# Kernel tuning notes

Hardware: AMD Instinct MI355X
Metric: run time of the kernel (lower is better)

The kernel has to match this reference:

```python
import jax, jax.numpy as jnp
from jax import lax
import numpy as np

B, C, O, NF, H, W = 4, 64, 64, 64, 128, 128
DK = 3
K = DK * DK
PAD = DK // 2


def setup_inputs() -> dict:
    key = jax.random.key(0)
    k0, k1, k2, k3 = jax.random.split(key, 4)
    inputs = jax.random.normal(k0, (B, C, H, W), jnp.float32)
    feat = jax.random.normal(k1, (B, NF, H, W), jnp.float32)
    # small offset-conv weights keep learned offsets in a realistic sub-pixel range
    om_w = jax.random.normal(k2, (C * 3 * K, NF, 3, 3), jnp.float32) * 0.02
    om_b = jnp.zeros((C * 3 * K,), jnp.float32)
    dc_w = jax.random.normal(k3, (O, C, DK, DK), jnp.float32) * (1.0 / np.sqrt(C * K))
    dc_b = jnp.zeros((O,), jnp.float32)
    return dict(inputs=inputs, feat=feat, om_w=om_w, om_b=om_b, dc_w=dc_w, dc_b=dc_b)


def _gather(img, y, x):
    # img: [B,C,H,W]; y,x: int32 [B,C,K,H,W]; zero outside bounds
    valid = (y >= 0) & (y < H) & (x >= 0) & (x < W)
    yc = jnp.clip(y, 0, H - 1)
    xc = jnp.clip(x, 0, W - 1)
    idx = (yc * W + xc).reshape(B, C, K, H * W)
    flat = img.reshape(B, C, 1, H * W)
    v = jnp.take_along_axis(flat, idx, axis=3).reshape(B, C, K, H, W)
    return jnp.where(valid, v, 0.0)


def _forward(inputs, feat, om_w, om_b, dc_w, dc_b):
    # offset/mask conv: nf -> in_nc*3*K, 3x3, pad 1
    off_msk = lax.conv_general_dilated(
        feat, om_w, (1, 1), ((1, 1), (1, 1)),
        dimension_numbers=('NCHW', 'OIHW', 'NCHW')) + om_b[None, :, None, None]
    # offsets interleaved (y,x) per kernel tap per deformable group (= channel)
    off = off_msk[:, :C * 2 * K].reshape(B, C, K, 2, H, W)
    msk = jax.nn.sigmoid(off_msk[:, C * 2 * K:]).reshape(B, C, K, H, W)

    ky = (jnp.arange(K) // DK - PAD).astype(jnp.float32)  # [K]
    kx = (jnp.arange(K) % DK - PAD).astype(jnp.float32)
    hg = jnp.arange(H, dtype=jnp.float32)
    wg = jnp.arange(W, dtype=jnp.float32)
    py = hg[None, None, None, :, None] + ky[None, None, :, None, None] + off[:, :, :, 0]  # [B,C,K,H,W]
    px = wg[None, None, None, None, :] + kx[None, None, :, None, None] + off[:, :, :, 1]

    y0f = jnp.floor(py); x0f = jnp.floor(px)
    wy = py - y0f; wx = px - x0f
    y0 = y0f.astype(jnp.int32); x0 = x0f.astype(jnp.int32)
    y1 = y0 + 1; x1 = x0 + 1

    v00 = _gather(inputs, y0, x0)
    v01 = _gather(inputs, y0, x1)
    v10 = _gather(inputs, y1, x0)
    v11 = _gather(inputs, y1, x1)
    sampled = ((1 - wy) * (1 - wx) * v00 + (1 - wy) * wx * v01
               + wy * (1 - wx) * v10 + wy * wx * v11) * msk  # [B,C,K,H,W]

    out = jnp.einsum('bckhw,ock->bohw', sampled, dc_w.reshape(O, C, K))
    out = out + dc_b[None, :, None, None]
    return jax.nn.relu(out)


def reference(inputs, feat, om_w, om_b, dc_w, dc_b):
    return _forward(inputs, feat, om_w, om_b, dc_w, dc_b)
```

## Files before the change

kernel.cpp:

```cpp
#include <hip/hip_runtime.h>
#include <hip/hip_bf16.h>

typedef __bf16 bf16;
typedef __bf16 bf16x8 __attribute__((ext_vector_type(8)));
typedef __bf16 bf16x4 __attribute__((ext_vector_type(4)));
typedef float f32x4 __attribute__((ext_vector_type(4)));
typedef float f32x2 __attribute__((ext_vector_type(2)));
typedef float f32x2u __attribute__((ext_vector_type(2))) __attribute__((aligned(4)));
typedef int  i32x4 __attribute__((ext_vector_type(4)));

#define MFMA16(a, b, c) __builtin_amdgcn_mfma_f32_16x16x32_bf16((a), (b), (c), 0, 0, 0)

static constexpr size_t FEATS_OFF = 0;
static constexpr size_t OMW3_OFF  = 8388608;
static constexpr size_t DCW_OFF   = OMW3_OFF + 1990656;
static constexpr size_t SC_OFF    = DCW_OFF + 73728;
static constexpr size_t PAD_OFF   = SC_OFF + 9216;


__global__ void prep_featS(const float* __restrict__ feat, bf16* __restrict__ featS) {
    const int hh = blockIdx.x, b = blockIdx.y;
    __shared__ float t[64][129];
    for (int i = threadIdx.x; i < 64 * 32; i += 256) {
        int cf = i >> 5, q = i & 31;
        const float* src = feat + ((size_t)(b * 64 + cf) * 128 + hh) * 128 + q * 4;
        t[cf][q * 4 + 0] = src[0];
        t[cf][q * 4 + 1] = src[1];
        t[cf][q * 4 + 2] = src[2];
        t[cf][q * 4 + 3] = src[3];
    }
    __syncthreads();
    for (int i = threadIdx.x; i < 1024; i += 256) {
        int px = i >> 3, cfb = i & 7;
        int sb = cfb ^ (px & 7);
        bf16x8 v;
#pragma unroll
        for (int e = 0; e < 8; ++e) v[e] = (bf16)t[cfb * 8 + e][px];
        *(bf16x8*)(featS + ((size_t)((b * 128 + hh) * 128 + px) << 6) + sb * 8) = v;
    }
}

__global__ void prep_weights(const float* __restrict__ om_w, const float* __restrict__ om_b,
                             const float* __restrict__ dc_w,
                             bf16* __restrict__ omw3, bf16* __restrict__ dcw2p,
                             float* __restrict__ scf) {
    int i = blockIdx.x * 256 + threadIdx.x;
    if (i < 995328) {
        int e = i & 511, lane = e >> 3, j = e & 7;
        int q = i >> 9;
        int t = q % 3, q2 = q / 3, kk = q2 % 18, ct = q2 / 18;
        int ck = ct * 16 + (lane & 15);
        int kcol = kk * 32 + (lane >> 4) * 8 + j;
        int tap = kcol >> 6, cf = kcol & 63;
        int ch = (t < 2) ? (ck * 2 + t) : (1152 + ck);
        omw3[i] = (bf16)om_w[ch * 576 + cf * 9 + tap];
    }
    if (i < 36864) {
        int j = i & 7, lane = (i >> 3) & 63, ot = (i >> 9) & 3, win = i >> 11;
        int o = ot * 16 + (lane & 15);
        int ck = win * 32 + (lane >> 4) * 8 + j;
        dcw2p[i] = (bf16)dc_w[o * 576 + ck];
    }
    if (i < 576) {
        int ck = i;
        int c = ck / 9, kd = ck - 9 * c, kq = kd / 3, kx = kd - 3 * kq;
        int pr = ck >> 1, lo = ck & 1;
        scf[pr * 8 + 0 + lo] = om_b[ck * 2]     + (float)(kq + 2);
        scf[pr * 8 + 2 + lo] = om_b[ck * 2 + 1] + (float)(kx + 2);
        scf[pr * 8 + 4 + lo] = om_b[1152 + ck];
        scf[pr * 8 + 6 + lo] = __uint_as_float((unsigned)(c * 17956));
    }
}

__global__ void prep_pad(const float* __restrict__ inputs, float* __restrict__ pad) {
    int yy = blockIdx.x, bc = blockIdx.y, xx = threadIdx.x;
    if (xx >= 134) return;
    float v = 0.f;
    if (yy >= 3 && yy <= 130 && xx >= 3 && xx <= 130)
        v = inputs[(size_t)bc * 16384 + (yy - 3) * 128 + (xx - 3)];
    pad[((size_t)bc * 134 + yy) * 134 + xx] = v;
}


__global__ void __launch_bounds__(256, 3)
deform_fused(const float* __restrict__ pad,
             const bf16* __restrict__ featS,
             const bf16* __restrict__ omw3,
             const bf16* __restrict__ dcw2p,
             const f32x4* __restrict__ sconst,
             const float* __restrict__ dcb,
             float* __restrict__ out)
{
    const int bid = blockIdx.x;
    const int P0 = (bid & 1) << 6;
    const int h = (bid >> 1) & 127;
    const int b = bid >> 8;
    const int tid = threadIdx.x;
    const int lane = tid & 63;
    const int wid_s = __builtin_amdgcn_readfirstlane(tid >> 6);
    const int l15 = lane & 15, g = lane >> 4;

    __shared__ __align__(16) unsigned char smem[41728];
    char* featB = (char*)smem;
    char* bufA  = (char*)smem + 25344;
    char* bufB  = (char*)smem + 33536;

    for (int i = tid; i < 6336; i += 256) ((unsigned*)featB)[i] = 0u;
    __syncthreads();
    {
        const int s0 = (P0 == 0) ? 0 : 63;
        const int q0 = (P0 == 0) ? 1 : 0;
        for (int i = tid; i < 1560; i += 256) {
            int ky = i / 520, rem = i - ky * 520, row = rem >> 3, c = rem & 7;
            int hh = h - 1 + ky;
            if ((unsigned)hh < 128u) {
                const char* src = (const char*)featS
                    + (((size_t)(b * 128 + hh) * 128 + s0 + row) << 7) + c * 16;
                *(i32x4*)(featB + ((ky * 66 + q0 + row) << 7) + c * 16) = *(const i32x4*)src;
            }
        }
    }
    __syncthreads();

    int fb9[9];
#pragma unroll
    for (int tap = 0; tap < 9; ++tap) {
        const int kyp = tap / 3, kxp = tap - 3 * kyp;
        const int q = l15 + kxp;
        fb9[tap] = (kyp * 66 + q) * 128 + ((g ^ ((q + 7) & 7)) << 4);
    }

    f32x4 acc2[4];
#pragma unroll
    for (int u = 0; u < 4; ++u) acc2[u] = (f32x4){0.f, 0.f, 0.f, 0.f};

    const bf16* omw3_l = omw3 + lane * 8;
    const bf16* dcw_l  = dcw2p + lane * 8;
    const float* padb0 = pad + (size_t)b * 64 * 17956;
    const f32x2 hb2 = {(float)h, (float)h};
    const f32x2 fx2 = {(float)(P0 + l15), (float)(P0 + l15)};
    const int g4 = g * 4;
    const int rswz = (g ^ (l15 & 7)) << 4;
    const int wswz = ((wid_s * 4 + g) ^ ((l15 & 7) << 1)) << 3;

#pragma unroll 1
    for (int blk = 0; blk < 9; ++blk) {
        char* bcur  = (blk & 1) ? bufB : bufA;
        char* bprev = (blk & 1) ? bufA : bufB;

        if (blk > 0) {
            bf16x8 aK0 = *(const bf16x8*)(dcw_l + (((blk - 1) * 8 + wid_s) << 9));
            bf16x8 aK1 = *(const bf16x8*)(dcw_l + (((blk - 1) * 8 + 4 + wid_s) << 9));
            __builtin_amdgcn_s_setprio(1);
#pragma unroll
            for (int u = 0; u < 4; ++u) {
                const int rb = (u * 16 + l15) * 128 + rswz;
                bf16x8 b0 = *(const bf16x8*)(bprev + rb);
                bf16x8 b1 = *(const bf16x8*)(bprev + (rb ^ 64));
                acc2[u] = MFMA16(aK0, b0, acc2[u]);
                acc2[u] = MFMA16(aK1, b1, acc2[u]);
            }
            __builtin_amdgcn_s_setprio(0);
        }

        f32x4 acc1[3][4];
#pragma unroll
        for (int t = 0; t < 3; ++t)
#pragma unroll
            for (int nf = 0; nf < 4; ++nf) acc1[t][nf] = (f32x4){0.f, 0.f, 0.f, 0.f};

        const int abase = (blk * 4 + wid_s) * 27648;
#pragma unroll
        for (int kk = 0; kk < 18; ++kk) {
            bf16x8 a0 = *(const bf16x8*)(omw3_l + abase + ((kk * 3 + 0) << 9));
            bf16x8 a1 = *(const bf16x8*)(omw3_l + abase + ((kk * 3 + 1) << 9));
            bf16x8 a2 = *(const bf16x8*)(omw3_l + abase + ((kk * 3 + 2) << 9));
            const int base = fb9[kk >> 1] ^ ((kk & 1) << 6);
            bf16x8 bfr[4];
#pragma unroll
            for (int nf = 0; nf < 4; ++nf)
                bfr[nf] = *(const bf16x8*)(featB + base + nf * 2048);
            __builtin_amdgcn_s_setprio(1);
#pragma unroll
            for (int nf = 0; nf < 4; ++nf) {
                acc1[0][nf] = MFMA16(a0, bfr[nf], acc1[0][nf]);
                acc1[1][nf] = MFMA16(a1, bfr[nf], acc1[1][nf]);
                acc1[2][nf] = MFMA16(a2, bfr[nf], acc1[2][nf]);
            }
            __builtin_amdgcn_s_setprio(0);
        }

        const f32x4* scB = sconst + (blk * 64 + wid_s * 16);
        f32x4 e0A = scB[g4 + 0], e1A = scB[g4 + 1];
        f32x4 e0B = scB[g4 + 2], e1B = scB[g4 + 3];
        f32x2 yb[2], xb[2], mb[2];
        unsigned co[2][2];
        yb[0] = f32x2{e0A.x, e0A.y} + hb2;
        xb[0] = f32x2{e0A.z, e0A.w} + fx2;
        mb[0] = f32x2{e1A.x, e1A.y};
        co[0][0] = __float_as_uint(e1A.z); co[0][1] = __float_as_uint(e1A.w);
        yb[1] = f32x2{e0B.x, e0B.y} + hb2;
        xb[1] = f32x2{e0B.z, e0B.w} + fx2;
        mb[1] = f32x2{e1B.x, e1B.y};
        co[1][0] = __float_as_uint(e1B.z); co[1][1] = __float_as_uint(e1B.w);

#pragma unroll
        for (int nf = 0; nf < 4; ++nf) {
            float s[4];
#pragma unroll
            for (int pi = 0; pi < 2; ++pi) {
                f32x2 py = f32x2{acc1[0][nf][2 * pi], acc1[0][nf][2 * pi + 1]} + yb[pi];
                f32x2 px = f32x2{acc1[1][nf][2 * pi], acc1[1][nf][2 * pi + 1]} + xb[pi];
                f32x2 lg = f32x2{acc1[2][nf][2 * pi], acc1[2][nf][2 * pi + 1]} + mb[pi];
#pragma unroll
                for (int e = 0; e < 2; ++e) {
                    float pyc = __builtin_amdgcn_fmed3f(py[e], 0.5f, 132.5f);
                    float pxc = __builtin_amdgcn_fmed3f(px[e], 0.5f, 132.5f);
                    int y0 = (int)pyc, x0 = (int)pxc;
                    float wy = __builtin_amdgcn_fractf(pyc);
                    float wx = __builtin_amdgcn_fractf(pxc);
                    unsigned off = co[pi][e] + (unsigned)(y0 * 134 + x0);
                    f32x2u t0 = *(const f32x2u*)(padb0 + off);
                    f32x2u t1 = *(const f32x2u*)(padb0 + off + 134);
                    float top = t0.x + wx * (t0.y - t0.x);
                    float bot = t1.x + wx * (t1.y - t1.x);
                    float bil = top + wy * (bot - top);
                    float mk = __builtin_amdgcn_rcpf(1.f + __expf(-lg[e]));
                    s[2 * pi + e] = bil * mk;
                }
            }
            bf16x4 pk4 = {(bf16)s[0], (bf16)s[1], (bf16)s[2], (bf16)s[3]};
            *(bf16x4*)(bcur + (nf * 16 + l15) * 128 + wswz) = pk4;
            xb[0] += 16.f; xb[1] += 16.f;
        }
        __syncthreads();
    }

    {
        bf16x8 aK0 = *(const bf16x8*)(dcw_l + ((8 * 8 + wid_s) << 9));
        bf16x8 aK1 = *(const bf16x8*)(dcw_l + ((8 * 8 + 4 + wid_s) << 9));
#pragma unroll
        for (int u = 0; u < 4; ++u) {
            const int rb = (u * 16 + l15) * 128 + rswz;
            bf16x8 b0 = *(const bf16x8*)(bufA + rb);
            bf16x8 b1 = *(const bf16x8*)(bufA + (rb ^ 64));
            acc2[u] = MFMA16(aK0, b0, acc2[u]);
            acc2[u] = MFMA16(aK1, b1, acc2[u]);
        }
    }

    float bias[4];
#pragma unroll
    for (int r = 0; r < 4; ++r) bias[r] = dcb[wid_s * 16 + g * 4 + r];
#pragma unroll
    for (int u = 0; u < 4; ++u)
#pragma unroll
        for (int r = 0; r < 4; ++r) {
            int o = wid_s * 16 + g * 4 + r;
            out[((size_t)(b * 64 + o) * 128 + h) * 128 + P0 + u * 16 + l15]
                = fmaxf(acc2[u][r] + bias[r], 0.f);
        }
}

extern "C" void kernel_launch(void* const* d_in, const int* in_sizes, int n_in,
                              void* d_out, int out_size, void* d_ws, size_t ws_size,
                              hipStream_t stream) {
    const float* inputs = (const float*)d_in[0];
    const float* feat   = (const float*)d_in[1];
    const float* om_w   = (const float*)d_in[2];
    const float* om_b   = (const float*)d_in[3];
    const float* dc_w   = (const float*)d_in[4];
    const float* dc_b   = (const float*)d_in[5];
    float* out = (float*)d_out;

    char* ws = (char*)d_ws;
    bf16*  featS  = (bf16*)(ws + FEATS_OFF);
    bf16*  omw3   = (bf16*)(ws + OMW3_OFF);
    bf16*  dcw2p  = (bf16*)(ws + DCW_OFF);
    float* scf    = (float*)(ws + SC_OFF);
    float* pad    = (float*)(ws + PAD_OFF);

    prep_featS<<<dim3(128, 4), 256, 0, stream>>>(feat, featS);
    prep_weights<<<(995328 + 255) / 256, 256, 0, stream>>>(om_w, om_b, dc_w, omw3, dcw2p, scf);
    prep_pad<<<dim3(134, 256), 256, 0, stream>>>(inputs, pad);

    deform_fused<<<1024, 256, 0, stream>>>(pad, featS, omw3, dcw2p,
                                           (const f32x4*)scf, dc_b, out);
}
```

Baseline: 204.8 us.

## Read zero-padded feature halo directly from global memory instead of LDS staging

The prep kernel now writes a spatially zero-padded (130x130) bf16 channel-last feature tensor. The fused kernel drops its per-block LDS staging of the 3-row halo and loads the offset-conv B operands straight from global memory. That removes the LDS fill, the zeroing pass and two barriers, and shrinks shared memory enough to raise the launch bound to 4 blocks per SU. The cost is that the 18x4 inner-loop fragment loads now go to global/L2, which has higher latency than LDS and no swizzle, so the MFMA loop may stall on memory.

After: 755.7 us. 269% more time.

```diff
diff --git a/kernel.cpp b/kernel.cpp
--- a/kernel.cpp
+++ b/kernel.cpp
@@ -7,36 +7,44 @@
 typedef float f32x4 __attribute__((ext_vector_type(4)));
 typedef float f32x2 __attribute__((ext_vector_type(2)));
 typedef float f32x2u __attribute__((ext_vector_type(2))) __attribute__((aligned(4)));
-typedef int  i32x4 __attribute__((ext_vector_type(4)));
 
 #define MFMA16(a, b, c) __builtin_amdgcn_mfma_f32_16x16x32_bf16((a), (b), (c), 0, 0, 0)
 
-static constexpr size_t FEATS_OFF = 0;
-static constexpr size_t OMW3_OFF  = 8388608;
-static constexpr size_t DCW_OFF   = OMW3_OFF + 1990656;
-static constexpr size_t SC_OFF    = DCW_OFF + 73728;
-static constexpr size_t PAD_OFF   = SC_OFF + 9216;
-
-
-__global__ void prep_featS(const float* __restrict__ feat, bf16* __restrict__ featS) {
+static constexpr size_t FEATSP_OFF = 0;
+static constexpr size_t OMW_OFF    = 8652800;
+static constexpr size_t DCW_OFF    = OMW_OFF + 1990656;
+static constexpr size_t SC_OFF     = DCW_OFF + 73728;
+static constexpr size_t PAD_OFF    = SC_OFF + 9216;
+
+
+__global__ void prep_featSP(const float* __restrict__ feat, bf16* __restrict__ featSP) {
     const int hh = blockIdx.x, b = blockIdx.y;
+    bf16* dst = featSP + (size_t)(b * 130 + hh) * 130 * 64;
+    if (hh == 0 || hh == 129) {
+        for (int i = threadIdx.x; i < 4160; i += 256) ((unsigned*)dst)[i] = 0u;
+        return;
+    }
     __shared__ float t[64][129];
     for (int i = threadIdx.x; i < 64 * 32; i += 256) {
         int cf = i >> 5, q = i & 31;
-        const float* src = feat + ((size_t)(b * 64 + cf) * 128 + hh) * 128 + q * 4;
+        const float* src = feat + ((size_t)(b * 64 + cf) * 128 + (hh - 1)) * 128 + q * 4;
         t[cf][q * 4 + 0] = src[0];
         t[cf][q * 4 + 1] = src[1];
         t[cf][q * 4 + 2] = src[2];
         t[cf][q * 4 + 3] = src[3];
     }
     __syncthreads();
-    for (int i = threadIdx.x; i < 1024; i += 256) {
-        int px = i >> 3, cfb = i & 7;
-        int sb = cfb ^ (px & 7);
+    for (int i = threadIdx.x; i < 1040; i += 256) {
+        int pc = i >> 3, cfb = i & 7;
         bf16x8 v;
-#pragma unroll
-        for (int e = 0; e < 8; ++e) v[e] = (bf16)t[cfb * 8 + e][px];
-        *(bf16x8*)(featS + ((size_t)((b * 128 + hh) * 128 + px) << 6) + sb * 8) = v;
+        if (pc == 0 || pc == 129) {
+#pragma unroll
+            for (int e = 0; e < 8; ++e) v[e] = (bf16)0.f;
+        } else {
+#pragma unroll
+            for (int e = 0; e < 8; ++e) v[e] = (bf16)t[cfb * 8 + e][pc - 1];
+        }
+        *(bf16x8*)(dst + pc * 64 + cfb * 8) = v;
     }
 }
 
@@ -82,9 +90,9 @@
 }
 
 
-__global__ void __launch_bounds__(256, 3)
+__global__ void __launch_bounds__(256, 4)
 deform_fused(const float* __restrict__ pad,
-             const bf16* __restrict__ featS,
+             const bf16* __restrict__ featSP,
              const bf16* __restrict__ omw3,
              const bf16* __restrict__ dcw2p,
              const f32x4* __restrict__ sconst,
@@ -100,35 +108,9 @@
     const int wid_s = __builtin_amdgcn_readfirstlane(tid >> 6);
     const int l15 = lane & 15, g = lane >> 4;
 
-    __shared__ __align__(16) unsigned char smem[41728];
-    char* featB = (char*)smem;
-    char* bufA  = (char*)smem + 25344;
-    char* bufB  = (char*)smem + 33536;
-
-    for (int i = tid; i < 6336; i += 256) ((unsigned*)featB)[i] = 0u;
-    __syncthreads();
-    {
-        const int s0 = (P0 == 0) ? 0 : 63;
-        const int q0 = (P0 == 0) ? 1 : 0;
-        for (int i = tid; i < 1560; i += 256) {
-            int ky = i / 520, rem = i - ky * 520, row = rem >> 3, c = rem & 7;
-            int hh = h - 1 + ky;
-            if ((unsigned)hh < 128u) {
-                const char* src = (const char*)featS
-                    + (((size_t)(b * 128 + hh) * 128 + s0 + row) << 7) + c * 16;
-                *(i32x4*)(featB + ((ky * 66 + q0 + row) << 7) + c * 16) = *(const i32x4*)src;
-            }
-        }
-    }
-    __syncthreads();
-
-    int fb9[9];
-#pragma unroll
-    for (int tap = 0; tap < 9; ++tap) {
-        const int kyp = tap / 3, kxp = tap - 3 * kyp;
-        const int q = l15 + kxp;
-        fb9[tap] = (kyp * 66 + q) * 128 + ((g ^ ((q + 7) & 7)) << 4);
-    }
+    __shared__ __align__(16) unsigned char smem[16384];
+    char* bufA = (char*)smem;
+    char* bufB = (char*)smem + 8192;
 
     f32x4 acc2[4];
 #pragma unroll
@@ -137,6 +119,8 @@
     const bf16* omw3_l = omw3 + lane * 8;
     const bf16* dcw_l  = dcw2p + lane * 8;
     const float* padb0 = pad + (size_t)b * 64 * 17956;
+    const char* fbase = (const char*)featSP
+        + (((size_t)(b * 130 + h) * 130 + P0 + l15) << 7) + g * 16;
     const f32x2 hb2 = {(float)h, (float)h};
     const f32x2 fx2 = {(float)(P0 + l15), (float)(P0 + l15)};
     const int g4 = g * 4;
@@ -172,14 +156,16 @@
         const int abase = (blk * 4 + wid_s) * 27648;
 #pragma unroll
         for (int kk = 0; kk < 18; ++kk) {
+            const int tap = kk >> 1;
+            const int kyp = tap / 3, kxp = tap - 3 * kyp;
+            const int foff = ((kyp * 130 + kxp) << 7) + (kk & 1) * 64;
             bf16x8 a0 = *(const bf16x8*)(omw3_l + abase + ((kk * 3 + 0) << 9));
             bf16x8 a1 = *(const bf16x8*)(omw3_l + abase + ((kk * 3 + 1) << 9));
             bf16x8 a2 = *(const bf16x8*)(omw3_l + abase + ((kk * 3 + 2) << 9));
-            const int base = fb9[kk >> 1] ^ ((kk & 1) << 6);
             bf16x8 bfr[4];
 #pragma unroll
             for (int nf = 0; nf < 4; ++nf)
-                bfr[nf] = *(const bf16x8*)(featB + base + nf * 2048);
+                bfr[nf] = *(const bf16x8*)(fbase + foff + nf * 2048);
             __builtin_amdgcn_s_setprio(1);
 #pragma unroll
             for (int nf = 0; nf < 4; ++nf) {
@@ -274,16 +260,16 @@
     float* out = (float*)d_out;
 
     char* ws = (char*)d_ws;
-    bf16*  featS  = (bf16*)(ws + FEATS_OFF);
-    bf16*  omw3   = (bf16*)(ws + OMW3_OFF);
+    bf16*  featSP = (bf16*)(ws + FEATSP_OFF);
+    bf16*  omw3   = (bf16*)(ws + OMW_OFF);
     bf16*  dcw2p  = (bf16*)(ws + DCW_OFF);
     float* scf    = (float*)(ws + SC_OFF);
     float* pad    = (float*)(ws + PAD_OFF);
 
-    prep_featS<<<dim3(128, 4), 256, 0, stream>>>(feat, featS);
+    prep_featSP<<<dim3(130, 4), 256, 0, stream>>>(feat, featSP);
     prep_weights<<<(995328 + 255) / 256, 256, 0, stream>>>(om_w, om_b, dc_w, omw3, dcw2p, scf);
     prep_pad<<<dim3(134, 256), 256, 0, stream>>>(inputs, pad);
 
-    deform_fused<<<1024, 256, 0, stream>>>(pad, featS, omw3, dcw2p,
+    deform_fused<<<1024, 256, 0, stream>>>(pad, featSP, omw3, dcw2p,
                                            (const f32x4*)scf, dc_b, out);
 }
```
